# Kernel tuning notes

Hardware: AMD Instinct MI355X
Metric: run time of the kernel (lower is better)

The kernel has to match this reference:

```python
import jax, jax.numpy as jnp
import numpy as np

B, N, DIN, DOUT = 32, 1024, 256, 256


def setup_inputs() -> dict:
    key = jax.random.key(0)
    ks = jax.random.split(key, 7)
    s = 1.0 / np.sqrt(DIN)
    return {
        "x": jax.random.normal(ks[0], (B, N, DIN), dtype=jnp.float32),
        "Wq": jax.random.uniform(ks[1], (DOUT, DIN), minval=-s, maxval=s, dtype=jnp.float32),
        "bq": jax.random.uniform(ks[2], (DOUT,), minval=-s, maxval=s, dtype=jnp.float32),
        "Wk": jax.random.uniform(ks[3], (DOUT, DIN), minval=-s, maxval=s, dtype=jnp.float32),
        "bk": jax.random.uniform(ks[4], (DOUT,), minval=-s, maxval=s, dtype=jnp.float32),
        "Wv": jax.random.uniform(ks[5], (DOUT, DIN), minval=-s, maxval=s, dtype=jnp.float32),
        "bv": jax.random.uniform(ks[6], (DOUT,), minval=-s, maxval=s, dtype=jnp.float32),
    }


def reference(x, Wq, bq, Wk, bk, Wv, bv):
    # q, k, v: (B, N, Dout)
    q = jnp.einsum("bnd,od->bno", x, Wq) + bq
    k = jnp.einsum("bnd,od->bno", x, Wk) + bk
    v = jnp.einsum("bnd,od->bno", x, Wv) + bv
    # logits: (B, N, N) = q @ k^T per batch
    logits = jnp.einsum("bnd,bmd->bnm", q, k)
    # NOTE: softmax over the BATCH dim (axis=0), as in the original module
    attn = jax.nn.softmax(logits, axis=0)
    out = jnp.einsum("bnm,bmd->bnd", attn, v)  # (B, N, Dout)
    return out
```

## Files before the change

### kernel.cpp

```cpp
#include <hip/hip_runtime.h>

typedef __bf16 bf16x8 __attribute__((ext_vector_type(8)));
typedef __bf16 bf16x4 __attribute__((ext_vector_type(4)));
typedef float  f32x4  __attribute__((ext_vector_type(4)));

#define BM 128
#define BN 128
#define BK 64

__device__ __forceinline__ void g2l16(const void* g, void* l) {
    __builtin_amdgcn_global_load_lds((const __attribute__((address_space(1))) void*)g,
                                     (__attribute__((address_space(3))) void*)l, 16, 0, 0);
}

template<int EPI, int FLAT>
__global__ __launch_bounds__(256)
void gemm_nt(const __bf16* __restrict__ A, const __bf16* __restrict__ B,
             void* __restrict__ Cv, const float* __restrict__ bias,
             int lda, int ldb, int ldc, int K,
             long sA, long sB, long sC)
{
    __shared__ __align__(16) __bf16 As[BM * BK];
    __shared__ __align__(16) __bf16 Bs[BN * BK];

    const int tid  = threadIdx.x;
    const int w    = tid >> 6;
    const int lane = tid & 63;
    const int quad = lane >> 4;
    const int l16  = lane & 15;
    const int wm   = w & 1;
    const int wn   = w >> 1;

    int m0, n0, z;
    if constexpr (FLAT) {
        const int id = blockIdx.x;
        z = id & 31;
        const int xy = id >> 5;
        m0 = (xy & 7) * BM;
        n0 = (xy >> 3) * BN;
    } else {
        m0 = blockIdx.x * BM;
        n0 = blockIdx.y * BN;
        z  = blockIdx.z;
    }

    const __bf16* Ab = A + (size_t)z * sA;
    const __bf16* Bb = B + (size_t)z * sB;

    const int srow = (w << 3) + (lane >> 3);
    const int scol = ((lane & 7) ^ (lane >> 3)) << 3;
    char* ldsA = (char*)As + (size_t)w * 1024;
    char* ldsB = (char*)Bs + (size_t)w * 1024;

    const __bf16* Ag = Ab + (size_t)(m0 + srow) * lda + scol;
    const __bf16* Bg = Bb + (size_t)(n0 + srow) * ldb + scol;

    f32x4 acc[4][4] = {};

    for (int k0 = 0; k0 < K; k0 += BK) {
        __syncthreads();
        #pragma unroll
        for (int c = 0; c < 4; c++)
            g2l16(Ag + (size_t)(c * 32) * lda + k0, ldsA + c * 4096);
        #pragma unroll
        for (int c = 0; c < 4; c++)
            g2l16(Bg + (size_t)(c * 32) * ldb + k0, ldsB + c * 4096);
        __syncthreads();

        #pragma unroll
        for (int kk = 0; kk < BK; kk += 32) {
            const int ub = kk >> 3;
            bf16x8 a[4], b[4];
            #pragma unroll
            for (int mt = 0; mt < 4; mt++) {
                const int row = wm * 64 + mt * 16 + l16;
                const int cp  = ((quad + ub) ^ (row & 7)) << 3;
                a[mt] = *(const bf16x8*)&As[row * BK + cp];
            }
            #pragma unroll
            for (int nt = 0; nt < 4; nt++) {
                const int row = wn * 64 + nt * 16 + l16;
                const int cp  = ((quad + ub) ^ (row & 7)) << 3;
                b[nt] = *(const bf16x8*)&Bs[row * BK + cp];
            }
            #pragma unroll
            for (int mt = 0; mt < 4; mt++)
                #pragma unroll
                for (int nt = 0; nt < 4; nt++)
                    acc[mt][nt] = __builtin_amdgcn_mfma_f32_16x16x32_bf16(
                        a[mt], b[nt], acc[mt][nt], 0, 0, 0);
        }
    }

    #pragma unroll
    for (int mt = 0; mt < 4; mt++) {
        const int mb = m0 + wm * 64 + mt * 16 + quad * 4;
        #pragma unroll
        for (int nt = 0; nt < 4; nt++) {
            const int n = n0 + wn * 64 + nt * 16 + l16;
            if constexpr (EPI == 2) {
                __bf16* C = (__bf16*)Cv + (size_t)z * sC;
                #pragma unroll
                for (int r = 0; r < 4; r++)
                    C[(size_t)(mb + r) * ldc + n] = (__bf16)__expf(acc[mt][nt][r]);
            } else {
                const float bn = bias[z * 256 + n];
                if (z < 2) {
                    __bf16* C = (__bf16*)Cv + (size_t)z * sC;
                    #pragma unroll
                    for (int r = 0; r < 4; r++)
                        C[(size_t)(mb + r) * ldc + n] = (__bf16)(acc[mt][nt][r] + bn);
                } else {
                    __bf16* C = (__bf16*)Cv + 2 * sC;
                    const int bidx = mb >> 10, mloc = mb & 1023;
                    bf16x4 pk;
                    #pragma unroll
                    for (int r = 0; r < 4; r++) pk[r] = (__bf16)(acc[mt][nt][r] + bn);
                    *(bf16x4*)(C + (size_t)bidx * 262144 + (size_t)n * 1024 + mloc) = pk;
                }
            }
        }
    }
}

__global__ __launch_bounds__(256)
void gemm_pv(const __bf16* __restrict__ E, const float* __restrict__ Srcp,
             const __bf16* __restrict__ vT, float* __restrict__ out)
{
    __shared__ __align__(16) __bf16 As[128 * 64];
    __shared__ __align__(16) __bf16 Bs[128 * 64];

    const int tid  = threadIdx.x;
    const int w    = tid >> 6;
    const int lane = tid & 63;
    const int quad = lane >> 4;
    const int l16  = lane & 15;
    const int wm   = w & 1;
    const int wn   = w >> 1;

    const int id = blockIdx.x;
    const int z  = id & 31;
    const int xy = id >> 5;
    const int m0 = (xy & 7) * 128;
    const int n0 = (xy >> 3) * 128;

    const __bf16* Eb = E  + (size_t)z * 1048576;
    const __bf16* Vb = vT + (size_t)z * 262144;
    float*        Ob = out + (size_t)z * 262144;

    const int srow = (w << 3) + (lane >> 3);
    const int scol = ((lane & 7) ^ (lane >> 3)) << 3;
    char* ldsB = (char*)Bs + (size_t)w * 1024;
    const __bf16* Bg = Vb + (size_t)(n0 + srow) * 1024 + scol;

    const int arow = tid >> 1;
    const int auh  = (tid & 1) * 4;
    const __bf16* Ag = Eb + (size_t)(m0 + arow) * 1024;
    const float*  Sg = Srcp + (size_t)(m0 + arow) * 1024;
    __bf16* Ad = As + arow * 64;

    f32x4 acc[4][4] = {};

    for (int k0 = 0; k0 < 1024; k0 += BK) {
        __syncthreads();
        #pragma unroll
        for (int c = 0; c < 4; c++)
            g2l16(Bg + (size_t)(c * 32) * 1024 + k0, ldsB + c * 4096);
        #pragma unroll
        for (int s = 0; s < 4; s++) {
            const int u   = auh + s;
            const int col = k0 + u * 8;
            bf16x8 e  = *(const bf16x8*)(Ag + col);
            f32x4  r0 = *(const f32x4*)(Sg + col);
            f32x4  r1 = *(const f32x4*)(Sg + col + 4);
            bf16x8 en;
            en[0] = (__bf16)((float)e[0] * r0[0]);
            en[1] = (__bf16)((float)e[1] * r0[1]);
            en[2] = (__bf16)((float)e[2] * r0[2]);
            en[3] = (__bf16)((float)e[3] * r0[3]);
            en[4] = (__bf16)((float)e[4] * r1[0]);
            en[5] = (__bf16)((float)e[5] * r1[1]);
            en[6] = (__bf16)((float)e[6] * r1[2]);
            en[7] = (__bf16)((float)e[7] * r1[3]);
            *(bf16x8*)(Ad + ((u ^ (arow & 7)) << 3)) = en;
        }
        __syncthreads();

        #pragma unroll
        for (int kk = 0; kk < BK; kk += 32) {
            const int ub = kk >> 3;
            bf16x8 a[4], b[4];
            #pragma unroll
            for (int mt = 0; mt < 4; mt++) {
                const int row = wm * 64 + mt * 16 + l16;
                const int cp  = ((quad + ub) ^ (row & 7)) << 3;
                a[mt] = *(const bf16x8*)&As[row * BK + cp];
            }
            #pragma unroll
            for (int nt = 0; nt < 4; nt++) {
                const int row = wn * 64 + nt * 16 + l16;
                const int cp  = ((quad + ub) ^ (row & 7)) << 3;
                b[nt] = *(const bf16x8*)&Bs[row * BK + cp];
            }
            #pragma unroll
            for (int mt = 0; mt < 4; mt++)
                #pragma unroll
                for (int nt = 0; nt < 4; nt++)
                    acc[mt][nt] = __builtin_amdgcn_mfma_f32_16x16x32_bf16(
                        a[mt], b[nt], acc[mt][nt], 0, 0, 0);
        }
    }

    #pragma unroll
    for (int mt = 0; mt < 4; mt++) {
        const int mb = m0 + wm * 64 + mt * 16 + quad * 4;
        #pragma unroll
        for (int nt = 0; nt < 4; nt++) {
            const int n = n0 + wn * 64 + nt * 16 + l16;
            #pragma unroll
            for (int r = 0; r < 4; r++)
                Ob[(size_t)(mb + r) * 256 + n] = acc[mt][nt][r];
        }
    }
}

__global__ __launch_bounds__(256)
void cvt_all(const float* __restrict__ x,
             const float* __restrict__ Wq, const float* __restrict__ Wk,
             const float* __restrict__ Wv,
             const float* __restrict__ bq, const float* __restrict__ bk,
             const float* __restrict__ bv,
             __bf16* __restrict__ xb, __bf16* __restrict__ Wqb,
             float* __restrict__ bpack)
{
    const int i = blockIdx.x * 256 + threadIdx.x;
    if (i < 1073152) {
        const float* s; __bf16* d; int off;
        if (i < 1048576)      { s = x;  d = xb;            off = i; }
        else if (i < 1056768) { s = Wq; d = Wqb;           off = i - 1048576; }
        else if (i < 1064960) { s = Wk; d = Wqb + 131072;  off = i - 1056768; }
        else                  { s = Wv; d = Wqb + 262144;  off = i - 1064960; }
        const float4* s4 = (const float4*)s;
        const float4 f0 = s4[off * 2], f1 = s4[off * 2 + 1];
        bf16x8 o;
        o[0] = (__bf16)f0.x; o[1] = (__bf16)f0.y; o[2] = (__bf16)f0.z; o[3] = (__bf16)f0.w;
        o[4] = (__bf16)f1.x; o[5] = (__bf16)f1.y; o[6] = (__bf16)f1.z; o[7] = (__bf16)f1.w;
        ((bf16x8*)d)[off] = o;
    } else if (i < 1073344) {
        const int j = i - 1073152;
        const int sel = j >> 6, jj = j & 63;
        const float* s = sel == 0 ? bq : (sel == 1 ? bk : bv);
        ((float4*)bpack)[j] = ((const float4*)s)[jj];
    }
}

__global__ __launch_bounds__(256)
void reduce_s(const __bf16* __restrict__ E, float* __restrict__ Srcp)
{
    const size_t p = (size_t)blockIdx.x * 256 + threadIdx.x;
    const bf16x8* E8 = (const bf16x8*)E;
    float s[8] = {0.f, 0.f, 0.f, 0.f, 0.f, 0.f, 0.f, 0.f};
    #pragma unroll
    for (int b = 0; b < 32; b++) {
        bf16x8 e = E8[(size_t)b * 131072 + p];
        #pragma unroll
        for (int j = 0; j < 8; j++) s[j] += (float)e[j];
    }
    f32x4 r0, r1;
    #pragma unroll
    for (int j = 0; j < 4; j++) r0[j] = __builtin_amdgcn_rcpf(s[j]);
    #pragma unroll
    for (int j = 0; j < 4; j++) r1[j] = __builtin_amdgcn_rcpf(s[j + 4]);
    ((f32x4*)Srcp)[p * 2]     = r0;
    ((f32x4*)Srcp)[p * 2 + 1] = r1;
}

extern "C" void kernel_launch(void* const* d_in, const int* in_sizes, int n_in,
                              void* d_out, int out_size, void* d_ws, size_t ws_size,
                              hipStream_t stream)
{
    const float* x  = (const float*)d_in[0];
    const float* Wq = (const float*)d_in[1];
    const float* bq = (const float*)d_in[2];
    const float* Wk = (const float*)d_in[3];
    const float* bk = (const float*)d_in[4];
    const float* Wv = (const float*)d_in[5];
    const float* bv = (const float*)d_in[6];
    float* out = (float*)d_out;

    char* ws = (char*)d_ws;
    float*  Srcp  = (float*) (ws);
    __bf16* xb    = (__bf16*)(ws);
    __bf16* qkv   = (__bf16*)(ws + (16u << 20));
    __bf16* E     = (__bf16*)(ws + (64u << 20));
    __bf16* Wqb   = (__bf16*)(ws + (128u << 20));
    float*  bpack = (float*) (ws + (128u << 20) + (3u << 18));

    cvt_all<<<4194, 256, 0, stream>>>(x, Wq, Wk, Wv, bq, bk, bv, xb, Wqb, bpack);

    gemm_nt<4, 0><<<dim3(256, 2, 3), 256, 0, stream>>>(xb, Wqb, qkv, bpack,
                                                       256, 256, 256, 256,
                                                       0, 131072, 8388608);

    gemm_nt<2, 1><<<2048, 256, 0, stream>>>(qkv, qkv + 8388608, E, nullptr,
                                            256, 256, 1024, 256,
                                            262144, 262144, 1048576);

    reduce_s<<<512, 256, 0, stream>>>(E, Srcp);

    gemm_pv<<<512, 256, 0, stream>>>(E, Srcp, qkv + 2 * 8388608, out);
}
```

Measured before the change: 213.5 us.

## Normalize softmax in place and simplify PV GEMM with async loads and smaller tiles

The reduction kernel now keeps all 32 batch values in registers, computes reciprocal sums and writes normalized E back in place. This removes the fp32 reciprocal buffer and the per-tile rescaling inside the PV GEMM, which can now stream E into shared memory directly with global_load_lds. The PV GEMM switches to 128x64 tiles with twice as many blocks, and both the QK and PV kernels use a new block-to-batch mapping meant to change L2 locality. The cost is an extra bf16 write pass over E plus higher register pressure in the normalization kernel.

Measured after the change: 192.3 us. -9.9%, faster.

```diff
diff --git a/kernel.cpp b/kernel.cpp
--- a/kernel.cpp
+++ b/kernel.cpp
@@ -13,7 +13,7 @@
                                      (__attribute__((address_space(3))) void*)l, 16, 0, 0);
 }
 
-template<int EPI, int FLAT>
+template<int EPI, int SWZ>
 __global__ __launch_bounds__(256)
 void gemm_nt(const __bf16* __restrict__ A, const __bf16* __restrict__ B,
              void* __restrict__ Cv, const float* __restrict__ bias,
@@ -32,12 +32,13 @@
     const int wn   = w >> 1;
 
     int m0, n0, z;
-    if constexpr (FLAT) {
+    if constexpr (SWZ == 1) {
         const int id = blockIdx.x;
-        z = id & 31;
-        const int xy = id >> 5;
-        m0 = (xy & 7) * BM;
-        n0 = (xy >> 3) * BN;
+        const int x  = id & 7, s = id >> 3;
+        z = x + ((s >> 6) << 3);
+        const int t = s & 63;
+        m0 = (t & 7) * BM;
+        n0 = (t >> 3) * BN;
     } else {
         m0 = blockIdx.x * BM;
         n0 = blockIdx.y * BN;
@@ -124,11 +125,11 @@
 }
 
 __global__ __launch_bounds__(256)
-void gemm_pv(const __bf16* __restrict__ E, const float* __restrict__ Srcp,
-             const __bf16* __restrict__ vT, float* __restrict__ out)
+void gemm_pv(const __bf16* __restrict__ E, const __bf16* __restrict__ vT,
+             float* __restrict__ out)
 {
     __shared__ __align__(16) __bf16 As[128 * 64];
-    __shared__ __align__(16) __bf16 Bs[128 * 64];
+    __shared__ __align__(16) __bf16 Bs[64 * 64];
 
     const int tid  = threadIdx.x;
     const int w    = tid >> 6;
@@ -139,10 +140,11 @@
     const int wn   = w >> 1;
 
     const int id = blockIdx.x;
-    const int z  = id & 31;
-    const int xy = id >> 5;
-    const int m0 = (xy & 7) * 128;
-    const int n0 = (xy >> 3) * 128;
+    const int x  = id & 7, s = id >> 3;
+    const int z  = x + ((s >> 5) << 3);
+    const int t  = s & 31;
+    const int m0 = (t & 7) * 128;
+    const int n0 = (t >> 3) * 64;
 
     const __bf16* Eb = E  + (size_t)z * 1048576;
     const __bf16* Vb = vT + (size_t)z * 262144;
@@ -150,46 +152,28 @@
 
     const int srow = (w << 3) + (lane >> 3);
     const int scol = ((lane & 7) ^ (lane >> 3)) << 3;
+    char* ldsA = (char*)As + (size_t)w * 1024;
     char* ldsB = (char*)Bs + (size_t)w * 1024;
+
+    const __bf16* Ag = Eb + (size_t)(m0 + srow) * 1024 + scol;
     const __bf16* Bg = Vb + (size_t)(n0 + srow) * 1024 + scol;
 
-    const int arow = tid >> 1;
-    const int auh  = (tid & 1) * 4;
-    const __bf16* Ag = Eb + (size_t)(m0 + arow) * 1024;
-    const float*  Sg = Srcp + (size_t)(m0 + arow) * 1024;
-    __bf16* Ad = As + arow * 64;
-
-    f32x4 acc[4][4] = {};
+    f32x4 acc[4][2] = {};
 
     for (int k0 = 0; k0 < 1024; k0 += BK) {
         __syncthreads();
         #pragma unroll
         for (int c = 0; c < 4; c++)
+            g2l16(Ag + (size_t)(c * 32) * 1024 + k0, ldsA + c * 4096);
+        #pragma unroll
+        for (int c = 0; c < 2; c++)
             g2l16(Bg + (size_t)(c * 32) * 1024 + k0, ldsB + c * 4096);
-        #pragma unroll
-        for (int s = 0; s < 4; s++) {
-            const int u   = auh + s;
-            const int col = k0 + u * 8;
-            bf16x8 e  = *(const bf16x8*)(Ag + col);
-            f32x4  r0 = *(const f32x4*)(Sg + col);
-            f32x4  r1 = *(const f32x4*)(Sg + col + 4);
-            bf16x8 en;
-            en[0] = (__bf16)((float)e[0] * r0[0]);
-            en[1] = (__bf16)((float)e[1] * r0[1]);
-            en[2] = (__bf16)((float)e[2] * r0[2]);
-            en[3] = (__bf16)((float)e[3] * r0[3]);
-            en[4] = (__bf16)((float)e[4] * r1[0]);
-            en[5] = (__bf16)((float)e[5] * r1[1]);
-            en[6] = (__bf16)((float)e[6] * r1[2]);
-            en[7] = (__bf16)((float)e[7] * r1[3]);
-            *(bf16x8*)(Ad + ((u ^ (arow & 7)) << 3)) = en;
-        }
         __syncthreads();
 
         #pragma unroll
         for (int kk = 0; kk < BK; kk += 32) {
             const int ub = kk >> 3;
-            bf16x8 a[4], b[4];
+            bf16x8 a[4], b[2];
             #pragma unroll
             for (int mt = 0; mt < 4; mt++) {
                 const int row = wm * 64 + mt * 16 + l16;
@@ -197,15 +181,15 @@
                 a[mt] = *(const bf16x8*)&As[row * BK + cp];
             }
             #pragma unroll
-            for (int nt = 0; nt < 4; nt++) {
-                const int row = wn * 64 + nt * 16 + l16;
+            for (int nt = 0; nt < 2; nt++) {
+                const int row = wn * 32 + nt * 16 + l16;
                 const int cp  = ((quad + ub) ^ (row & 7)) << 3;
                 b[nt] = *(const bf16x8*)&Bs[row * BK + cp];
             }
             #pragma unroll
             for (int mt = 0; mt < 4; mt++)
                 #pragma unroll
-                for (int nt = 0; nt < 4; nt++)
+                for (int nt = 0; nt < 2; nt++)
                     acc[mt][nt] = __builtin_amdgcn_mfma_f32_16x16x32_bf16(
                         a[mt], b[nt], acc[mt][nt], 0, 0, 0);
         }
@@ -215,8 +199,8 @@
     for (int mt = 0; mt < 4; mt++) {
         const int mb = m0 + wm * 64 + mt * 16 + quad * 4;
         #pragma unroll
-        for (int nt = 0; nt < 4; nt++) {
-            const int n = n0 + wn * 64 + nt * 16 + l16;
+        for (int nt = 0; nt < 2; nt++) {
+            const int n = n0 + wn * 32 + nt * 16 + l16;
             #pragma unroll
             for (int r = 0; r < 4; r++)
                 Ob[(size_t)(mb + r) * 256 + n] = acc[mt][nt][r];
@@ -255,24 +239,28 @@
 }
 
 __global__ __launch_bounds__(256)
-void reduce_s(const __bf16* __restrict__ E, float* __restrict__ Srcp)
+void softmax_norm(__bf16* __restrict__ E)
 {
     const size_t p = (size_t)blockIdx.x * 256 + threadIdx.x;
-    const bf16x8* E8 = (const bf16x8*)E;
+    bf16x8* E8 = (bf16x8*)E;
+    bf16x8 e[32];
+    #pragma unroll
+    for (int b = 0; b < 32; b++) e[b] = E8[(size_t)b * 131072 + p];
     float s[8] = {0.f, 0.f, 0.f, 0.f, 0.f, 0.f, 0.f, 0.f};
     #pragma unroll
+    for (int b = 0; b < 32; b++)
+        #pragma unroll
+        for (int j = 0; j < 8; j++) s[j] += (float)e[b][j];
+    float rs[8];
+    #pragma unroll
+    for (int j = 0; j < 8; j++) rs[j] = __builtin_amdgcn_rcpf(s[j]);
+    #pragma unroll
     for (int b = 0; b < 32; b++) {
-        bf16x8 e = E8[(size_t)b * 131072 + p];
-        #pragma unroll
-        for (int j = 0; j < 8; j++) s[j] += (float)e[j];
-    }
-    f32x4 r0, r1;
-    #pragma unroll
-    for (int j = 0; j < 4; j++) r0[j] = __builtin_amdgcn_rcpf(s[j]);
-    #pragma unroll
-    for (int j = 0; j < 4; j++) r1[j] = __builtin_amdgcn_rcpf(s[j + 4]);
-    ((f32x4*)Srcp)[p * 2]     = r0;
-    ((f32x4*)Srcp)[p * 2 + 1] = r1;
+        bf16x8 o = e[b];
+        #pragma unroll
+        for (int j = 0; j < 8; j++) o[j] = (__bf16)((float)o[j] * rs[j]);
+        E8[(size_t)b * 131072 + p] = o;
+    }
 }
 
 extern "C" void kernel_launch(void* const* d_in, const int* in_sizes, int n_in,
@@ -289,7 +277,6 @@
     float* out = (float*)d_out;
 
     char* ws = (char*)d_ws;
-    float*  Srcp  = (float*) (ws);
     __bf16* xb    = (__bf16*)(ws);
     __bf16* qkv   = (__bf16*)(ws + (16u << 20));
     __bf16* E     = (__bf16*)(ws + (64u << 20));
@@ -306,7 +293,7 @@
                                             256, 256, 1024, 256,
                                             262144, 262144, 1048576);
 
-    reduce_s<<<512, 256, 0, stream>>>(E, Srcp);
-
-    gemm_pv<<<512, 256, 0, stream>>>(E, Srcp, qkv + 2 * 8388608, out);
-}
+    softmax_norm<<<512, 256, 0, stream>>>(E);
+
+    gemm_pv<<<1024, 256, 0, stream>>>(E, qkv + 2 * 8388608, out);
+}
```

## Narrow PV tile to 128x64 and remap block ids so batches stay per-XCD

Applied to the files above, without the earlier changes.

The logits GEMM and the PV GEMM now decode block ids so that all tiles of one batch share the same id&7 residue. With round-robin dispatch this keeps them on one XCD, so their shared operands can be reused in that XCD's L2. The PV GEMM output tile shrinks from 128x128 to 128x64 and its grid doubles to 1024 blocks, which gives more parallelism across the CUs. The cost is that each normalized E tile, including its Srcp scaling work, is now loaded and rescaled by four N-blocks instead of two.

Measured after the change: 254.1 us. +19.0%, slower.

```diff
diff --git a/kernel.cpp b/kernel.cpp
--- a/kernel.cpp
+++ b/kernel.cpp
@@ -13,7 +13,7 @@
                                      (__attribute__((address_space(3))) void*)l, 16, 0, 0);
 }
 
-template<int EPI, int FLAT>
+template<int EPI, int SWZ>
 __global__ __launch_bounds__(256)
 void gemm_nt(const __bf16* __restrict__ A, const __bf16* __restrict__ B,
              void* __restrict__ Cv, const float* __restrict__ bias,
@@ -32,12 +32,13 @@
     const int wn   = w >> 1;
 
     int m0, n0, z;
-    if constexpr (FLAT) {
+    if constexpr (SWZ == 1) {
         const int id = blockIdx.x;
-        z = id & 31;
-        const int xy = id >> 5;
-        m0 = (xy & 7) * BM;
-        n0 = (xy >> 3) * BN;
+        const int x  = id & 7, s = id >> 3;
+        z = x + ((s >> 6) << 3);
+        const int t = s & 63;
+        m0 = (t & 7) * BM;
+        n0 = (t >> 3) * BN;
     } else {
         m0 = blockIdx.x * BM;
         n0 = blockIdx.y * BN;
@@ -74,14 +75,12 @@
             #pragma unroll
             for (int mt = 0; mt < 4; mt++) {
                 const int row = wm * 64 + mt * 16 + l16;
-                const int cp  = ((quad + ub) ^ (row & 7)) << 3;
-                a[mt] = *(const bf16x8*)&As[row * BK + cp];
+                a[mt] = *(const bf16x8*)&As[row * BK + (((quad + ub) ^ (row & 7)) << 3)];
             }
             #pragma unroll
             for (int nt = 0; nt < 4; nt++) {
                 const int row = wn * 64 + nt * 16 + l16;
-                const int cp  = ((quad + ub) ^ (row & 7)) << 3;
-                b[nt] = *(const bf16x8*)&Bs[row * BK + cp];
+                b[nt] = *(const bf16x8*)&Bs[row * BK + (((quad + ub) ^ (row & 7)) << 3)];
             }
             #pragma unroll
             for (int mt = 0; mt < 4; mt++)
@@ -128,7 +127,7 @@
              const __bf16* __restrict__ vT, float* __restrict__ out)
 {
     __shared__ __align__(16) __bf16 As[128 * 64];
-    __shared__ __align__(16) __bf16 Bs[128 * 64];
+    __shared__ __align__(16) __bf16 Bs[64 * 64];
 
     const int tid  = threadIdx.x;
     const int w    = tid >> 6;
@@ -139,10 +138,11 @@
     const int wn   = w >> 1;
 
     const int id = blockIdx.x;
-    const int z  = id & 31;
-    const int xy = id >> 5;
-    const int m0 = (xy & 7) * 128;
-    const int n0 = (xy >> 3) * 128;
+    const int x  = id & 7, s = id >> 3;
+    const int z  = x + ((s >> 5) << 3);
+    const int t  = s & 31;
+    const int m0 = (t & 7) * 128;
+    const int n0 = (t >> 3) * 64;
 
     const __bf16* Eb = E  + (size_t)z * 1048576;
     const __bf16* Vb = vT + (size_t)z * 262144;
@@ -159,16 +159,16 @@
     const float*  Sg = Srcp + (size_t)(m0 + arow) * 1024;
     __bf16* Ad = As + arow * 64;
 
-    f32x4 acc[4][4] = {};
+    f32x4 acc[4][2] = {};
 
     for (int k0 = 0; k0 < 1024; k0 += BK) {
         __syncthreads();
         #pragma unroll
-        for (int c = 0; c < 4; c++)
+        for (int c = 0; c < 2; c++)
             g2l16(Bg + (size_t)(c * 32) * 1024 + k0, ldsB + c * 4096);
         #pragma unroll
-        for (int s = 0; s < 4; s++) {
-            const int u   = auh + s;
+        for (int s4 = 0; s4 < 4; s4++) {
+            const int u   = auh + s4;
             const int col = k0 + u * 8;
             bf16x8 e  = *(const bf16x8*)(Ag + col);
             f32x4  r0 = *(const f32x4*)(Sg + col);
@@ -189,23 +189,21 @@
         #pragma unroll
         for (int kk = 0; kk < BK; kk += 32) {
             const int ub = kk >> 3;
-            bf16x8 a[4], b[4];
+            bf16x8 a[4], b[2];
             #pragma unroll
             for (int mt = 0; mt < 4; mt++) {
                 const int row = wm * 64 + mt * 16 + l16;
-                const int cp  = ((quad + ub) ^ (row & 7)) << 3;
-                a[mt] = *(const bf16x8*)&As[row * BK + cp];
-            }
-            #pragma unroll
-            for (int nt = 0; nt < 4; nt++) {
-                const int row = wn * 64 + nt * 16 + l16;
-                const int cp  = ((quad + ub) ^ (row & 7)) << 3;
-                b[nt] = *(const bf16x8*)&Bs[row * BK + cp];
+                a[mt] = *(const bf16x8*)&As[row * BK + (((quad + ub) ^ (row & 7)) << 3)];
+            }
+            #pragma unroll
+            for (int nt = 0; nt < 2; nt++) {
+                const int row = wn * 32 + nt * 16 + l16;
+                b[nt] = *(const bf16x8*)&Bs[row * BK + (((quad + ub) ^ (row & 7)) << 3)];
             }
             #pragma unroll
             for (int mt = 0; mt < 4; mt++)
                 #pragma unroll
-                for (int nt = 0; nt < 4; nt++)
+                for (int nt = 0; nt < 2; nt++)
                     acc[mt][nt] = __builtin_amdgcn_mfma_f32_16x16x32_bf16(
                         a[mt], b[nt], acc[mt][nt], 0, 0, 0);
         }
@@ -215,8 +213,8 @@
     for (int mt = 0; mt < 4; mt++) {
         const int mb = m0 + wm * 64 + mt * 16 + quad * 4;
         #pragma unroll
-        for (int nt = 0; nt < 4; nt++) {
-            const int n = n0 + wn * 64 + nt * 16 + l16;
+        for (int nt = 0; nt < 2; nt++) {
+            const int n = n0 + wn * 32 + nt * 16 + l16;
             #pragma unroll
             for (int r = 0; r < 4; r++)
                 Ob[(size_t)(mb + r) * 256 + n] = acc[mt][nt][r];
@@ -308,5 +306,5 @@
 
     reduce_s<<<512, 256, 0, stream>>>(E, Srcp);
 
-    gemm_pv<<<512, 256, 0, stream>>>(E, Srcp, qkv + 2 * 8388608, out);
-}
+    gemm_pv<<<1024, 256, 0, stream>>>(E, Srcp, qkv + 2 * 8388608, out);
+}
```
